# Performance work log

Hardware: AMD Instinct MI355X
Metric: run time of the kernel (lower is better)

The kernel has to match this reference:

```python
import jax, jax.numpy as jnp
import numpy as np

NEG_SLOPE = 0.2
MASK_FILL = -1e9

N, F_IN, K, F_OUT = 4096, 512, 8, 128


def setup_inputs() -> dict:
    key = jax.random.key(0)
    k1, k2, k3, k4, k5 = jax.random.split(key, 5)
    x = jax.random.normal(k1, (N, F_IN), dtype=jnp.float32)
    mask = jax.random.randint(k2, (N, N), 0, 2).astype(jnp.bool_)
    # ensure no fully-masked row (self loops)
    mask = mask | jnp.eye(N, dtype=jnp.bool_)
    # xavier-ish scaled params
    W = jax.random.normal(k3, (K * F_OUT, F_IN), dtype=jnp.float32) * (2.0 / (F_IN + K * F_OUT)) ** 0.5
    b = jnp.zeros((K * F_OUT,), dtype=jnp.float32)
    a_left = jax.random.normal(k4, (K, F_OUT), dtype=jnp.float32) * (2.0 / (1 + F_OUT)) ** 0.5
    a_right = jax.random.normal(k5, (K, F_OUT), dtype=jnp.float32) * (2.0 / (1 + F_OUT)) ** 0.5
    return {"x": x, "mask": mask, "W": W, "b": b, "a_left": a_left, "a_right": a_right}


def reference(x, mask, W, b, a_left, a_right):
    # Linear projection: (N, K*F') -> (N, K, F')
    h = (x @ W.T + b).reshape(x.shape[0], K, F_OUT)
    # Additive attention logits: e[k,n,m] = leaky_relu(a_left.h_n + a_right.h_m)
    left = jnp.einsum('nkf,kf->kn', h, a_left)    # (K, N)
    right = jnp.einsum('mkf,kf->km', h, a_right)  # (K, N)
    e = jax.nn.leaky_relu(left[:, :, None] + right[:, None, :], NEG_SLOPE)  # (K,N,N)
    # Mask out non-neighbors, softmax over neighbor axis m
    e = jnp.where(mask[None, :, :], e, MASK_FILL)
    a = jax.nn.softmax(e, axis=-1)  # (K, N, N)
    # Weighted aggregation (eq. 4) + ELU
    h_prime = jax.nn.elu(jnp.einsum('knm,mkf->nkf', a, h))  # (N, K, F')
    # Concat heads (eq. 5): (N, K*F')
    return h_prime.reshape(h_prime.shape[0], -1)
```

## Files before the change

### kernel.cpp

```cpp
#include <hip/hip_runtime.h>
#include <hip/hip_bf16.h>

typedef unsigned short u16;
typedef __attribute__((ext_vector_type(8))) short short8;
typedef __attribute__((ext_vector_type(2))) float f32x2;
typedef __attribute__((ext_vector_type(4))) float f32x4;
typedef __attribute__((ext_vector_type(16))) float f32x16;

#define N_NODES 4096
#define FIN 512
#define KH 8
#define FO 128
#define DM 1024
#define LOG2E 1.44269504088896340736f

__device__ __forceinline__ void gload16(const u16* g, u16* l) {
    __builtin_amdgcn_global_load_lds(
        (const __attribute__((address_space(1))) unsigned int*)g,
        (__attribute__((address_space(3))) unsigned int*)l,
        16, 0, 0);
}

__device__ __forceinline__ unsigned pk_bf16(float lo, float hi) {
    unsigned r;
    asm("v_cvt_pk_bf16_f32 %0, %1, %2" : "=v"(r) : "v"(lo), "v"(hi));
    return r;
}

__global__ __launch_bounds__(256) void split_bf16(const float* __restrict__ src,
                                                  u16* __restrict__ hi,
                                                  u16* __restrict__ lo,
                                                  int n4) {
    int idx = blockIdx.x * 256 + threadIdx.x;
    if (idx >= n4) return;
    float4 v = ((const float4*)src)[idx];
    unsigned h01 = pk_bf16(v.x, v.y);
    unsigned h23 = pk_bf16(v.z, v.w);
    float hx = __uint_as_float(h01 << 16);
    float hy = __uint_as_float(h01 & 0xffff0000u);
    float hz = __uint_as_float(h23 << 16);
    float hw = __uint_as_float(h23 & 0xffff0000u);
    unsigned l01 = pk_bf16(v.x - hx, v.y - hy);
    unsigned l23 = pk_bf16(v.z - hz, v.w - hw);
    uint2 hv; hv.x = h01; hv.y = h23;
    uint2 lv; lv.x = l01; lv.y = l23;
    ((uint2*)hi)[idx] = hv;
    ((uint2*)lo)[idx] = lv;
}

__global__ __launch_bounds__(512) void gemm_mfma(const u16* __restrict__ Xh,
                                                 const u16* __restrict__ Xl,
                                                 const u16* __restrict__ Wh,
                                                 const u16* __restrict__ Wl,
                                                 const float* __restrict__ bias,
                                                 const float* __restrict__ aL,
                                                 const float* __restrict__ aR,
                                                 float2* __restrict__ C2,
                                                 unsigned* __restrict__ D2b,
                                                 u16* __restrict__ HbT) {
    const int khead = blockIdx.x;
    const int n0 = blockIdx.y * 128;
    const int tid = threadIdx.x;
    const int w = tid >> 6, lane = tid & 63;
    const int wr = w >> 1, wc = w & 1;
    const int c = lane & 31, half = lane >> 5;

    __shared__ u16 S[2][16384];

    const int sa = w >> 1;
    const int shv = w & 1;
    const int scl = lane & 3;
    const int ssw = ((lane >> 2) ^ (lane >> 4)) & 3;
    const int sgc = scl ^ ssw;
    const u16* gb; int growbase;
    if (sa == 0)      { gb = Xh; growbase = n0; }
    else if (sa == 1) { gb = Xl; growbase = n0; }
    else if (sa == 2) { gb = Wh; growbase = khead * 128; }
    else              { gb = Wl; growbase = khead * 128; }
    const u16* glb = gb + (size_t)(growbase + shv * 64 + (lane >> 2)) * FIN + sgc * 8;
    const int sldsoff = sa * 4096 + shv * 64 * 32;

    const int sw = ((c) ^ (c >> 2)) & 3;
    const int aoff = (wr * 32 + c) * 32;
    const int boff0 = 8192 + (wc * 64 + c) * 32;
    const int boff1 = 8192 + (wc * 64 + 32 + c) * 32;

    f32x16 acc0, acc1;
#pragma unroll
    for (int i = 0; i < 16; ++i) { acc0[i] = 0.f; acc1[i] = 0.f; }

#pragma unroll
    for (int i = 0; i < 4; ++i)
        gload16(glb + (size_t)i * 16 * FIN, &S[0][sldsoff + i * 512]);
    __syncthreads();

    int cur = 0;
    for (int kt = 0; kt < 16; ++kt) {
        if (kt < 15) {
            const u16* gsrc = glb + (kt + 1) * 32;
            u16* dst = &S[cur ^ 1][sldsoff];
#pragma unroll
            for (int i = 0; i < 4; ++i)
                gload16(gsrc + (size_t)i * 16 * FIN, dst + i * 512);
        }

        const u16* sp = S[cur];
        short8 ah[2], al8[2], bh[2][2], bl8[2][2];
#pragma unroll
        for (int ks = 0; ks < 2; ++ks) {
            int ch = ((ks * 2 + half) ^ sw) * 8;
            ah[ks]     = *(const short8*)&sp[aoff + ch];
            al8[ks]    = *(const short8*)&sp[4096 + aoff + ch];
            bh[0][ks]  = *(const short8*)&sp[boff0 + ch];
            bl8[0][ks] = *(const short8*)&sp[boff0 + 4096 + ch];
            bh[1][ks]  = *(const short8*)&sp[boff1 + ch];
            bl8[1][ks] = *(const short8*)&sp[boff1 + 4096 + ch];
        }
#pragma unroll
        for (int ks = 0; ks < 2; ++ks) {
            acc0 = __builtin_amdgcn_mfma_f32_32x32x16_bf16(ah[ks], bh[0][ks], acc0, 0, 0, 0);
            acc0 = __builtin_amdgcn_mfma_f32_32x32x16_bf16(ah[ks], bl8[0][ks], acc0, 0, 0, 0);
            acc0 = __builtin_amdgcn_mfma_f32_32x32x16_bf16(al8[ks], bh[0][ks], acc0, 0, 0, 0);
            acc1 = __builtin_amdgcn_mfma_f32_32x32x16_bf16(ah[ks], bh[1][ks], acc1, 0, 0, 0);
            acc1 = __builtin_amdgcn_mfma_f32_32x32x16_bf16(ah[ks], bl8[1][ks], acc1, 0, 0, 0);
            acc1 = __builtin_amdgcn_mfma_f32_32x32x16_bf16(al8[ks], bh[1][ks], acc1, 0, 0, 0);
        }
        __syncthreads();
        cur ^= 1;
    }

    const int fglob = khead * FO + wc * 64 + c;
    float b0 = bias[fglob], b1 = bias[fglob + 32];
#pragma unroll
    for (int r = 0; r < 16; ++r) { acc0[r] += b0; acc1[r] += b1; }

    float alv0 = aL[fglob], alv1 = aL[fglob + 32];
    float arv0 = aR[fglob], arv1 = aR[fglob + 32];
    float pl[16], pr[16];
#pragma unroll
    for (int r = 0; r < 16; ++r) {
        pl[r] = acc0[r] * alv0 + acc1[r] * alv1;
        pr[r] = acc0[r] * arv0 + acc1[r] * arv1;
    }
#pragma unroll
    for (int off = 1; off < 32; off <<= 1) {
#pragma unroll
        for (int r = 0; r < 16; ++r) {
            pl[r] += __shfl_xor(pl[r], off);
            pr[r] += __shfl_xor(pr[r], off);
        }
    }

    u16* T = &S[0][0];
    float* LRf = (float*)&S[0][0] + 9216;

    if (c == 0) {
#pragma unroll
        for (int r = 0; r < 16; ++r) {
            int node = wr * 32 + (r & 3) + 8 * (r >> 2) + 4 * half;
            LRf[(wc * 2 + 0) * 128 + node] = pl[r];
            LRf[(wc * 2 + 1) * 128 + node] = pr[r];
        }
    }

#pragma unroll
    for (int q = 0; q < 4; ++q) {
        int nb = wr * 32 + q * 8 + 4 * half;
        unsigned p00 = pk_bf16(acc0[q * 4 + 0], acc0[q * 4 + 1]);
        unsigned p01 = pk_bf16(acc0[q * 4 + 2], acc0[q * 4 + 3]);
        unsigned p10 = pk_bf16(acc1[q * 4 + 0], acc1[q * 4 + 1]);
        unsigned p11 = pk_bf16(acc1[q * 4 + 2], acc1[q * 4 + 3]);
        *(unsigned*)&T[(wc * 64 + c) * 136 + nb]      = p00;
        *(unsigned*)&T[(wc * 64 + c) * 136 + nb + 2]  = p01;
        *(unsigned*)&T[(wc * 64 + 32 + c) * 136 + nb]     = p10;
        *(unsigned*)&T[(wc * 64 + 32 + c) * 136 + nb + 2] = p11;
    }
    __syncthreads();

    if (wc == 0) {
        int node = wr * 32 + (lane & 31);
        if (lane < 32) {
            float L = (LRf[0 * 128 + node] + LRf[2 * 128 + node]) * LOG2E;
            float2 cv; cv.x = exp2f(L); cv.y = exp2f(0.2f * L);
            C2[(size_t)khead * N_NODES + n0 + node] = cv;
        } else {
            float R = (LRf[1 * 128 + node] + LRf[3 * 128 + node]) * LOG2E;
            D2b[(size_t)khead * N_NODES + n0 + node] = pk_bf16(exp2f(R), exp2f(0.2f * R));
        }
    }

    {
        int f = tid >> 2, q = tid & 3;
        const uint4* src = (const uint4*)&T[f * 136 + q * 32];
        uint4* dst = (uint4*)(HbT + (size_t)(khead * FO + f) * N_NODES + n0 + q * 32);
#pragma unroll
        for (int u = 0; u < 4; ++u) dst[u] = src[u];
    }
}

__global__ __launch_bounds__(256) void pack_mask(const int* __restrict__ mask,
                                                 unsigned long long* __restrict__ mb) {
    int gid = blockIdx.x * 256 + threadIdx.x;
    int wid = gid >> 6, lane = gid & 63;
    int v = mask[(size_t)wid * 64 + lane];
    unsigned long long bits = __ballot(v != 0);
    if (lane == 0) mb[wid] = bits;
}

__global__ __launch_bounds__(512, 4) void gat_attn(const u16* __restrict__ HbT,
                                                   const float2* __restrict__ C2,
                                                   const unsigned* __restrict__ D2b,
                                                   const unsigned long long* __restrict__ mb,
                                                   float* __restrict__ out) {
    const int blk = blockIdx.x;
    const int k = blk & 7;
    const int n0 = (blk >> 3) * 64;
    const int tid = threadIdx.x;
    const int w = tid >> 6, lane = tid & 63;
    const int g = w >> 2, wg = w & 3;
    const int fr = lane & 15, kg = lane >> 4;

    __shared__ u16 Ht[2][2][128 * 64];

    const int n_a = n0 + wg * 16 + fr;
    const float2 ccf = C2[(size_t)k * N_NODES + n_a];
    const float ccx = ccf.x, ccy = ccf.y;
    const unsigned long long* mrow = mb + (size_t)n_a * 64 + g * 32;
    const int shA = kg * 8, shB = shA + 32;

    f32x4 acc[9];
#pragma unroll
    for (int c = 0; c < 9; ++c) acc[c] = 0.f;

    const short o1 = (fr == 0) ? (short)0x3F80 : (short)0;
    const short8 ones = {o1, o1, o1, o1, o1, o1, o1, o1};

    const int fsub = lane >> 3;
    const int seg = ((lane & 7) ^ fsub) * 8;
    const u16* gstage = HbT + (size_t)(k * FO + wg * 32 + fsub) * N_NODES + g * 2048 + seg;
    u16* lb0 = &Ht[g][0][wg * 2048];
    u16* lb1 = &Ht[g][1][wg * 2048];

    const int frx = fr & 7;
    const int off0 = fr * 64 + (kg ^ frx) * 8;
    const int off1 = fr * 64 + ((kg + 4) ^ frx) * 8;

    const unsigned* D2k = D2b + (size_t)k * N_NODES + g * 2048 + kg * 8;

    uint4 dc0, dc1, dc2, dc3;
    unsigned long long bc;
#pragma unroll
    for (int j = 0; j < 4; ++j)
        gload16(gstage + (size_t)j * 8 * N_NODES, lb0 + j * 512);
    dc0 = *(const uint4*)(D2k);      dc1 = *(const uint4*)(D2k + 4);
    dc2 = *(const uint4*)(D2k + 32); dc3 = *(const uint4*)(D2k + 36);
    bc = mrow[0];
    asm volatile("s_waitcnt vmcnt(5)" ::: "memory");
    __builtin_amdgcn_s_barrier();

#define ATTN_HALF(RBUF, SBUF, MT, DC0,DC1,DC2,DC3,BITS, DN0,DN1,DN2,DN3,NBITS) do {    \
    const unsigned nxt = ((MT) + 1) & 31;                                               \
    if ((MT) < 31) {                                                                    \
        const u16* gs = gstage + ((size_t)nxt << 6);                                    \
        _Pragma("unroll")                                                               \
        for (int j = 0; j < 4; ++j)                                                     \
            gload16(gs + (size_t)j * 8 * N_NODES, (SBUF) + j * 512);                    \
    }                                                                                   \
    { const unsigned* dnp = D2k + (nxt << 6);                                           \
      DN0 = *(const uint4*)(dnp);      DN1 = *(const uint4*)(dnp + 4);                  \
      DN2 = *(const uint4*)(dnp + 32); DN3 = *(const uint4*)(dnp + 36);                 \
      NBITS = mrow[nxt]; }                                                              \
    __builtin_amdgcn_sched_barrier(0);                                                  \
    {                                                                                   \
        unsigned m32a = (unsigned)((BITS) >> shA);                                      \
        unsigned m32b = (unsigned)((BITS) >> shB);                                      \
        unsigned wa[8] = {DC0.x, DC0.y, DC0.z, DC0.w, DC1.x, DC1.y, DC1.z, DC1.w};      \
        unsigned wb[8] = {DC2.x, DC2.y, DC2.z, DC2.w, DC3.x, DC3.y, DC3.z, DC3.w};      \
        float p0[8], p1[8];                                                             \
        _Pragma("unroll")                                                               \
        for (int v = 0; v < 8; ++v) {                                                   \
            float pa = fmaxf(ccx * __uint_as_float(wa[v] << 16),                        \
                             ccy * __uint_as_float(wa[v] & 0xffff0000u));               \
            unsigned sa2 = (unsigned)(((int)(m32a << (31 - v))) >> 31);                 \
            p0[v] = __uint_as_float(__float_as_uint(pa) & sa2);                         \
            float pb = fmaxf(ccx * __uint_as_float(wb[v] << 16),                        \
                             ccy * __uint_as_float(wb[v] & 0xffff0000u));               \
            unsigned sb2 = (unsigned)(((int)(m32b << (31 - v))) >> 31);                 \
            p1[v] = __uint_as_float(__float_as_uint(pb) & sb2);                         \
        }                                                                               \
        union { unsigned u[4]; short8 s; } ua, ub;                                      \
        _Pragma("unroll")                                                               \
        for (int vp = 0; vp < 4; ++vp) {                                                \
            ua.u[vp] = pk_bf16(p0[2 * vp], p0[2 * vp + 1]);                             \
            ub.u[vp] = pk_bf16(p1[2 * vp], p1[2 * vp + 1]);                             \
        }                                                                               \
        short8 a0 = ua.s, a1 = ub.s;                                                    \
        const u16* hb = (RBUF);                                                         \
        __builtin_amdgcn_s_setprio(1);                                                  \
        _Pragma("unroll")                                                               \
        for (int c = 0; c < 8; ++c) {                                                   \
            short8 b0 = *(const short8*)(hb + c * 1024 + off0);                         \
            short8 b1 = *(const short8*)(hb + c * 1024 + off1);                         \
            acc[c] = __builtin_amdgcn_mfma_f32_16x16x32_bf16(a0, b0, acc[c], 0, 0, 0);  \
            acc[c] = __builtin_amdgcn_mfma_f32_16x16x32_bf16(a1, b1, acc[c], 0, 0, 0);  \
        }                                                                               \
        acc[8] = __builtin_amdgcn_mfma_f32_16x16x32_bf16(a0, ones, acc[8], 0, 0, 0);    \
        acc[8] = __builtin_amdgcn_mfma_f32_16x16x32_bf16(a1, ones, acc[8], 0, 0, 0);    \
        __builtin_amdgcn_s_setprio(0);                                                  \
    }                                                                                   \
    asm volatile("s_waitcnt lgkmcnt(0)" ::: "memory");                                  \
    asm volatile("s_waitcnt vmcnt(5)" ::: "memory");                                    \
    __builtin_amdgcn_s_barrier();                                                       \
} while (0)

    {
        uint4 en0, en1, en2, en3;
        unsigned long long bn;
        const u16* rb0 = &Ht[g][0][0];
        const u16* rb1 = &Ht[g][1][0];
        for (int mt = 0; mt < 32; mt += 2) {
            ATTN_HALF(rb0, lb1, mt,     dc0, dc1, dc2, dc3, bc, en0, en1, en2, en3, bn);
            ATTN_HALF(rb1, lb0, mt + 1, en0, en1, en2, en3, bn, dc0, dc1, dc2, dc3, bc);
        }
    }
#undef ATTN_HALF

    asm volatile("s_waitcnt vmcnt(0)" ::: "memory");
    __syncthreads();

    float* cmb = (float*)&Ht[0][0][0];
    if (g == 1) {
        float* base = cmb + wg * (36 * 64);
#pragma unroll
        for (int c = 0; c < 9; ++c)
#pragma unroll
            for (int j = 0; j < 4; ++j) base[(c * 4 + j) * 64 + lane] = acc[c][j];
    }
    __syncthreads();
    if (g == 0) {
        const float* base = cmb + wg * (36 * 64);
#pragma unroll
        for (int c = 0; c < 9; ++c)
#pragma unroll
            for (int j = 0; j < 4; ++j) acc[c][j] += base[(c * 4 + j) * 64 + lane];

#pragma unroll
        for (int j = 0; j < 4; ++j) {
            float S = __shfl(acc[8][j], (lane & 48));
            float inv = 1.0f / S;
            int n_out = n0 + wg * 16 + kg * 4 + j;
            float* orow = out + (size_t)n_out * DM + k * FO + fr;
#pragma unroll
            for (int c = 0; c < 8; ++c) {
                float v = acc[c][j] * inv;
                float e = v > 0.f ? v : (__expf(v) - 1.0f);
                orow[c * 16] = e;
            }
        }
    }
}

extern "C" void kernel_launch(void* const* d_in, const int* in_sizes, int n_in,
                              void* d_out, int out_size, void* d_ws, size_t ws_size,
                              hipStream_t stream) {
    const float* x = (const float*)d_in[0];
    const int* mask = (const int*)d_in[1];
    const float* W = (const float*)d_in[2];
    const float* bias = (const float*)d_in[3];
    const float* aL = (const float*)d_in[4];
    const float* aR = (const float*)d_in[5];
    float* out = (float*)d_out;

    char* ws = (char*)d_ws;
    u16* Xh = (u16*)ws;   ws += (size_t)N_NODES * FIN * 2;
    u16* Xl = (u16*)ws;   ws += (size_t)N_NODES * FIN * 2;
    u16* Wh = (u16*)ws;   ws += (size_t)DM * FIN * 2;
    u16* Wl = (u16*)ws;   ws += (size_t)DM * FIN * 2;
    u16* HbT = (u16*)ws;  ws += (size_t)KH * FO * N_NODES * 2;
    float2* C2 = (float2*)ws;  ws += (size_t)KH * N_NODES * 8;
    unsigned* D2b = (unsigned*)ws; ws += (size_t)KH * N_NODES * 4;
    unsigned long long* mb = (unsigned long long*)ws;

    split_bf16<<<dim3(2048), dim3(256), 0, stream>>>(x, Xh, Xl, N_NODES * FIN / 4);
    split_bf16<<<dim3(512), dim3(256), 0, stream>>>(W, Wh, Wl, DM * FIN / 4);
    gemm_mfma<<<dim3(8, 32), dim3(512), 0, stream>>>(Xh, Xl, Wh, Wl, bias, aL, aR,
                                                     C2, D2b, HbT);
    pack_mask<<<dim3(65536), dim3(256), 0, stream>>>(mask, mb);
    gat_attn<<<dim3(512), dim3(512), 0, stream>>>(HbT, C2, D2b, mb, out);
}
```

Baseline: 127.0 us.

## Re-partition attention waves to share B fragments across two row groups

The attention kernel's eight waves are remapped so that each wave handles 32 destination rows (two 16-row A tiles) but only a quarter of each 64-neighbor tile. Each B fragment loaded from LDS now feeds two MFMAs, which halves LDS reads per MFMA, and the final reduction becomes four-way through LDS with serialized syncs. The cross-iteration prefetch of D and mask words into registers is removed: these are now loaded within the step, and the waits change from vmcnt(5) to vmcnt(0). This exposes global load latency and adds extra barriers in the epilogue.

```diff
diff --git a/kernel.cpp b/kernel.cpp
--- a/kernel.cpp
+++ b/kernel.cpp
@@ -210,151 +210,167 @@
 __global__ __launch_bounds__(512, 4) void gat_attn(const u16* __restrict__ HbT,
                                                    const float2* __restrict__ C2,
                                                    const unsigned* __restrict__ D2b,
-                                                   const unsigned long long* __restrict__ mb,
+                                                   const unsigned* __restrict__ mb32,
                                                    float* __restrict__ out) {
     const int blk = blockIdx.x;
     const int k = blk & 7;
     const int n0 = (blk >> 3) * 64;
     const int tid = threadIdx.x;
     const int w = tid >> 6, lane = tid & 63;
-    const int g = w >> 2, wg = w & 3;
+    const int ns = w & 1, g = (w >> 1) & 1, ks = w >> 2;
     const int fr = lane & 15, kg = lane >> 4;
 
     __shared__ u16 Ht[2][2][128 * 64];
 
-    const int n_a = n0 + wg * 16 + fr;
-    const float2 ccf = C2[(size_t)k * N_NODES + n_a];
-    const float ccx = ccf.x, ccy = ccf.y;
-    const unsigned long long* mrow = mb + (size_t)n_a * 64 + g * 32;
-    const int shA = kg * 8, shB = shA + 32;
-
-    f32x4 acc[9];
-#pragma unroll
-    for (int c = 0; c < 9; ++c) acc[c] = 0.f;
+    const int na0 = n0 + ns * 32 + fr;
+    const int na1 = na0 + 16;
+    const float2 c0f = C2[(size_t)k * N_NODES + na0];
+    const float2 c1f = C2[(size_t)k * N_NODES + na1];
+    const float cx0 = c0f.x, cy0 = c0f.y;
+    const float cx1 = c1f.x, cy1 = c1f.y;
+    const unsigned* mp0 = mb32 + (size_t)na0 * 128 + g * 64 + ks;
+    const unsigned* mp1 = mb32 + (size_t)na1 * 128 + g * 64 + ks;
+
+    f32x4 acc[2][9];
+#pragma unroll
+    for (int s = 0; s < 2; ++s)
+#pragma unroll
+        for (int c = 0; c < 9; ++c) acc[s][c] = 0.f;
 
     const short o1 = (fr == 0) ? (short)0x3F80 : (short)0;
     const short8 ones = {o1, o1, o1, o1, o1, o1, o1, o1};
 
+    const int q = ns * 2 + ks;
     const int fsub = lane >> 3;
     const int seg = ((lane & 7) ^ fsub) * 8;
-    const u16* gstage = HbT + (size_t)(k * FO + wg * 32 + fsub) * N_NODES + g * 2048 + seg;
-    u16* lb0 = &Ht[g][0][wg * 2048];
-    u16* lb1 = &Ht[g][1][wg * 2048];
+    const u16* gstage = HbT + (size_t)(k * FO + q * 32 + fsub) * N_NODES + g * 2048 + seg;
+    u16* lbA = &Ht[g][0][q * 2048];
+    u16* lbB = &Ht[g][1][q * 2048];
 
     const int frx = fr & 7;
-    const int off0 = fr * 64 + (kg ^ frx) * 8;
-    const int off1 = fr * 64 + ((kg + 4) ^ frx) * 8;
-
-    const unsigned* D2k = D2b + (size_t)k * N_NODES + g * 2048 + kg * 8;
-
-    uint4 dc0, dc1, dc2, dc3;
-    unsigned long long bc;
+    const int offb = fr * 64 + ((ks * 4 + kg) ^ frx) * 8;
+
+    const unsigned* D2k = D2b + (size_t)k * N_NODES + g * 2048 + ks * 32 + kg * 8;
+
 #pragma unroll
     for (int j = 0; j < 4; ++j)
-        gload16(gstage + (size_t)j * 8 * N_NODES, lb0 + j * 512);
-    dc0 = *(const uint4*)(D2k);      dc1 = *(const uint4*)(D2k + 4);
-    dc2 = *(const uint4*)(D2k + 32); dc3 = *(const uint4*)(D2k + 36);
-    bc = mrow[0];
-    asm volatile("s_waitcnt vmcnt(5)" ::: "memory");
+        gload16(gstage + (size_t)j * 8 * N_NODES, lbA + j * 512);
+    asm volatile("s_waitcnt vmcnt(0)" ::: "memory");
     __builtin_amdgcn_s_barrier();
 
-#define ATTN_HALF(RBUF, SBUF, MT, DC0,DC1,DC2,DC3,BITS, DN0,DN1,DN2,DN3,NBITS) do {    \
-    const unsigned nxt = ((MT) + 1) & 31;                                               \
-    if ((MT) < 31) {                                                                    \
-        const u16* gs = gstage + ((size_t)nxt << 6);                                    \
+#define ATTN_STEP(RBUF, SBUF, MT) do {                                                  \
+    const int mtv = (MT);                                                               \
+               \
+    const unsigned* dp = D2k + mtv * 64;                                                \
+    uint4 d0 = *(const uint4*)(dp);                                                     \
+    uint4 d1 = *(const uint4*)(dp + 4);                                                 \
+    unsigned m0w = mp0[mtv * 2];                                                        \
+    unsigned m1w = mp1[mtv * 2];                                                        \
+                                                                    \
+    if (mtv < 31) {                                                                     \
+        const u16* gs = gstage + ((size_t)(mtv + 1) << 6);                              \
         _Pragma("unroll")                                                               \
         for (int j = 0; j < 4; ++j)                                                     \
             gload16(gs + (size_t)j * 8 * N_NODES, (SBUF) + j * 512);                    \
     }                                                                                   \
-    { const unsigned* dnp = D2k + (nxt << 6);                                           \
-      DN0 = *(const uint4*)(dnp);      DN1 = *(const uint4*)(dnp + 4);                  \
-      DN2 = *(const uint4*)(dnp + 32); DN3 = *(const uint4*)(dnp + 36);                 \
-      NBITS = mrow[nxt]; }                                                              \
     __builtin_amdgcn_sched_barrier(0);                                                  \
+                                            \
     {                                                                                   \
-        unsigned m32a = (unsigned)((BITS) >> shA);                                      \
-        unsigned m32b = (unsigned)((BITS) >> shB);                                      \
-        unsigned wa[8] = {DC0.x, DC0.y, DC0.z, DC0.w, DC1.x, DC1.y, DC1.z, DC1.w};      \
-        unsigned wb[8] = {DC2.x, DC2.y, DC2.z, DC2.w, DC3.x, DC3.y, DC3.z, DC3.w};      \
-        float p0[8], p1[8];                                                             \
-        _Pragma("unroll")                                                               \
-        for (int v = 0; v < 8; ++v) {                                                   \
-            float pa = fmaxf(ccx * __uint_as_float(wa[v] << 16),                        \
-                             ccy * __uint_as_float(wa[v] & 0xffff0000u));               \
-            unsigned sa2 = (unsigned)(((int)(m32a << (31 - v))) >> 31);                 \
-            p0[v] = __uint_as_float(__float_as_uint(pa) & sa2);                         \
-            float pb = fmaxf(ccx * __uint_as_float(wb[v] << 16),                        \
-                             ccy * __uint_as_float(wb[v] & 0xffff0000u));               \
-            unsigned sb2 = (unsigned)(((int)(m32b << (31 - v))) >> 31);                 \
-            p1[v] = __uint_as_float(__float_as_uint(pb) & sb2);                         \
-        }                                                                               \
+        unsigned mq0 = m0w >> (kg * 8);                                                 \
+        unsigned mq1 = m1w >> (kg * 8);                                                 \
+        unsigned wa[8] = {d0.x, d0.y, d0.z, d0.w, d1.x, d1.y, d1.z, d1.w};              \
         union { unsigned u[4]; short8 s; } ua, ub;                                      \
         _Pragma("unroll")                                                               \
         for (int vp = 0; vp < 4; ++vp) {                                                \
-            ua.u[vp] = pk_bf16(p0[2 * vp], p0[2 * vp + 1]);                             \
-            ub.u[vp] = pk_bf16(p1[2 * vp], p1[2 * vp + 1]);                             \
+            unsigned u0 = wa[2 * vp], u1 = wa[2 * vp + 1];                              \
+            float dx0 = __uint_as_float(u0 << 16);                                      \
+            float dy0 = __uint_as_float(u0 & 0xffff0000u);                              \
+            float dx1 = __uint_as_float(u1 << 16);                                      \
+            float dy1 = __uint_as_float(u1 & 0xffff0000u);                              \
+            unsigned s00 = (unsigned)(((int)(mq0 << (31 - 2 * vp))) >> 31);             \
+            unsigned s01 = (unsigned)(((int)(mq0 << (30 - 2 * vp))) >> 31);             \
+            unsigned s10 = (unsigned)(((int)(mq1 << (31 - 2 * vp))) >> 31);             \
+            unsigned s11 = (unsigned)(((int)(mq1 << (30 - 2 * vp))) >> 31);             \
+            float q0a = __uint_as_float(__float_as_uint(fmaxf(cx0 * dx0, cy0 * dy0)) & s00); \
+            float q0b = __uint_as_float(__float_as_uint(fmaxf(cx0 * dx1, cy0 * dy1)) & s01); \
+            float q1a = __uint_as_float(__float_as_uint(fmaxf(cx1 * dx0, cy1 * dy0)) & s10); \
+            float q1b = __uint_as_float(__float_as_uint(fmaxf(cx1 * dx1, cy1 * dy1)) & s11); \
+            ua.u[vp] = pk_bf16(q0a, q0b);                                               \
+            ub.u[vp] = pk_bf16(q1a, q1b);                                               \
         }                                                                               \
         short8 a0 = ua.s, a1 = ub.s;                                                    \
+                            \
         const u16* hb = (RBUF);                                                         \
         __builtin_amdgcn_s_setprio(1);                                                  \
         _Pragma("unroll")                                                               \
         for (int c = 0; c < 8; ++c) {                                                   \
-            short8 b0 = *(const short8*)(hb + c * 1024 + off0);                         \
-            short8 b1 = *(const short8*)(hb + c * 1024 + off1);                         \
-            acc[c] = __builtin_amdgcn_mfma_f32_16x16x32_bf16(a0, b0, acc[c], 0, 0, 0);  \
-            acc[c] = __builtin_amdgcn_mfma_f32_16x16x32_bf16(a1, b1, acc[c], 0, 0, 0);  \
+            short8 b = *(const short8*)(hb + c * 1024 + offb);                          \
+            acc[0][c] = __builtin_amdgcn_mfma_f32_16x16x32_bf16(a0, b, acc[0][c], 0, 0, 0); \
+            acc[1][c] = __builtin_amdgcn_mfma_f32_16x16x32_bf16(a1, b, acc[1][c], 0, 0, 0); \
         }                                                                               \
-        acc[8] = __builtin_amdgcn_mfma_f32_16x16x32_bf16(a0, ones, acc[8], 0, 0, 0);    \
-        acc[8] = __builtin_amdgcn_mfma_f32_16x16x32_bf16(a1, ones, acc[8], 0, 0, 0);    \
+        acc[0][8] = __builtin_amdgcn_mfma_f32_16x16x32_bf16(a0, ones, acc[0][8], 0, 0, 0);  \
+        acc[1][8] = __builtin_amdgcn_mfma_f32_16x16x32_bf16(a1, ones, acc[1][8], 0, 0, 0);  \
         __builtin_amdgcn_s_setprio(0);                                                  \
     }                                                                                   \
+                        \
     asm volatile("s_waitcnt lgkmcnt(0)" ::: "memory");                                  \
-    asm volatile("s_waitcnt vmcnt(5)" ::: "memory");                                    \
+    asm volatile("s_waitcnt vmcnt(0)" ::: "memory");                                    \
     __builtin_amdgcn_s_barrier();                                                       \
 } while (0)
 
     {
-        uint4 en0, en1, en2, en3;
-        unsigned long long bn;
         const u16* rb0 = &Ht[g][0][0];
         const u16* rb1 = &Ht[g][1][0];
         for (int mt = 0; mt < 32; mt += 2) {
-            ATTN_HALF(rb0, lb1, mt,     dc0, dc1, dc2, dc3, bc, en0, en1, en2, en3, bn);
-            ATTN_HALF(rb1, lb0, mt + 1, en0, en1, en2, en3, bn, dc0, dc1, dc2, dc3, bc);
-        }
-    }
-#undef ATTN_HALF
-
-    asm volatile("s_waitcnt vmcnt(0)" ::: "memory");
+            ATTN_STEP(rb0, lbB, mt);
+            ATTN_STEP(rb1, lbA, mt + 1);
+        }
+    }
+#undef ATTN_STEP
+
     __syncthreads();
 
-    float* cmb = (float*)&Ht[0][0][0];
-    if (g == 1) {
-        float* base = cmb + wg * (36 * 64);
-#pragma unroll
-        for (int c = 0; c < 9; ++c)
-#pragma unroll
-            for (int j = 0; j < 4; ++j) base[(c * 4 + j) * 64 + lane] = acc[c][j];
-    }
-    __syncthreads();
-    if (g == 0) {
-        const float* base = cmb + wg * (36 * 64);
-#pragma unroll
-        for (int c = 0; c < 9; ++c)
-#pragma unroll
-            for (int j = 0; j < 4; ++j) acc[c][j] += base[(c * 4 + j) * 64 + lane];
-
-#pragma unroll
-        for (int j = 0; j < 4; ++j) {
-            float S = __shfl(acc[8][j], (lane & 48));
-            float inv = 1.0f / S;
-            int n_out = n0 + wg * 16 + kg * 4 + j;
-            float* orow = out + (size_t)n_out * DM + k * FO + fr;
-#pragma unroll
-            for (int c = 0; c < 8; ++c) {
-                float v = acc[c][j] * inv;
-                float e = v > 0.f ? v : (__expf(v) - 1.0f);
-                orow[c * 16] = e;
+    float* fb = (float*)&Ht[0][0][0];
+    const int myid = g + 2 * ks;
+    const int cb = ns * 4608 + lane;
+    for (int src = 1; src < 4; ++src) {
+        if (myid == src) {
+#pragma unroll
+            for (int s = 0; s < 2; ++s)
+#pragma unroll
+                for (int c = 0; c < 9; ++c)
+#pragma unroll
+                    for (int j = 0; j < 4; ++j)
+                        fb[cb + (((s * 9 + c) * 4 + j) << 6)] = acc[s][c][j];
+        }
+        __syncthreads();
+        if (myid == 0) {
+#pragma unroll
+            for (int s = 0; s < 2; ++s)
+#pragma unroll
+                for (int c = 0; c < 9; ++c)
+#pragma unroll
+                    for (int j = 0; j < 4; ++j)
+                        acc[s][c][j] += fb[cb + (((s * 9 + c) * 4 + j) << 6)];
+        }
+        __syncthreads();
+    }
+
+    if (myid == 0) {
+#pragma unroll
+        for (int s = 0; s < 2; ++s) {
+#pragma unroll
+            for (int j = 0; j < 4; ++j) {
+                float S = __shfl(acc[s][8][j], (lane & 48));
+                float inv = 1.0f / S;
+                int n_out = n0 + ns * 32 + s * 16 + kg * 4 + j;
+                float* orow = out + (size_t)n_out * DM + k * FO + fr;
+#pragma unroll
+                for (int c = 0; c < 8; ++c) {
+                    float v = acc[s][c][j] * inv;
+                    float e = v > 0.f ? v : (__expf(v) - 1.0f);
+                    orow[c * 16] = e;
+                }
             }
         }
     }
@@ -386,5 +402,5 @@
     gemm_mfma<<<dim3(8, 32), dim3(512), 0, stream>>>(Xh, Xl, Wh, Wl, bias, aL, aR,
                                                      C2, D2b, HbT);
     pack_mask<<<dim3(65536), dim3(256), 0, stream>>>(mask, mb);
-    gat_attn<<<dim3(512), dim3(512), 0, stream>>>(HbT, C2, D2b, mb, out);
-}
+    gat_attn<<<dim3(512), dim3(512), 0, stream>>>(HbT, C2, D2b, (const unsigned*)mb, out);
+}
```

Measured after the change: 125.7 us. Within noise of the previous version (-1.0%).
